# Optimization experiments

Measured on AMD Instinct MI355X. Metric: run time of the kernel, lower is better.

The kernel has to match this reference:

```python
import jax, jax.numpy as jnp
import numpy as np

BLOCKSIZE = 64
M = 8192  # out_features
N = 8192  # in_features

# bitsandbytes fp4 codebook (16 entries, normalized to [-1, 1])
FP4_CODE = np.array([0.0, 0.0052083333, 0.6666667, 1.0, 0.33333334, 0.5,
                     0.16666667, 0.25, 0.0, -0.0052083333, -0.6666667, -1.0,
                     -0.33333334, -0.5, -0.16666667, -0.25], dtype=np.float32)


def setup_inputs() -> dict:
    key = jax.random.key(0)
    k1, k2, k3, k4 = jax.random.split(key, 4)
    numel = M * N
    x = jax.random.normal(k1, (4, N), dtype=jnp.float32)
    # packed bytes: each byte holds two 4-bit codebook indices
    qweight = jax.random.randint(k2, (numel // 2,), 0, 256, dtype=jnp.int32)
    # per-block absmax scales (positive)
    absmax = jax.random.uniform(k3, (numel // BLOCKSIZE,), dtype=jnp.float32,
                                minval=0.01, maxval=1.0)
    code = jnp.asarray(FP4_CODE)
    bias = jax.random.normal(k4, (M,), dtype=jnp.float32)
    return {"x": x, "qweight": qweight, "absmax": absmax, "code": code, "bias": bias}


def _dequantize_fp4(qweight, absmax, code):
    # unpack two 4-bit indices per byte: high nibble first, low nibble second
    b = qweight.astype(jnp.int32)
    hi = (b >> 4) & 0xF
    lo = b & 0xF
    idx = jnp.stack([hi, lo], axis=-1).reshape(-1)          # [numel]
    vals = code[idx]                                        # codebook lookup
    # blockwise absmax scaling
    w = (vals.reshape(-1, BLOCKSIZE) * absmax[:, None]).reshape(M, N)
    return w


def reference(x, qweight, absmax, code, bias):
    w = _dequantize_fp4(qweight, absmax, code)              # [M, N]
    # nn.Linear semantics: y = x @ W^T + b
    return x @ w.T + bias
```

## Files before the change

kernel.cpp:

```cpp
#include <hip/hip_runtime.h>
#include <cstdint>

#define MDIM 8192
#define NDIM 8192
#define QPR  (NDIM / 2)
#define ABPR (NDIM / 64)
#define ROWS_PER_BLOCK 16
#define HGRAN 2048
#define NITER 32
#define RING 8

typedef _Float16 half2_t __attribute__((ext_vector_type(2)));
typedef uint32_t u32x4   __attribute__((ext_vector_type(4)));

__device__ __forceinline__ uint32_t f16bits(uint32_t idx) {
  uint32_t k  = idx & 7u;
  uint32_t hb = (uint32_t)(0x343138353C391D00ull >> (k * 8)) & 0xFFu;
  uint32_t lb = (0u - (hb & 1u)) & 0x55u;
  return (hb << 8) | lb | ((idx & 8u) << 12);
}

__device__ __forceinline__ uint32_t dec_pair(uint32_t b) {
  return f16bits((b >> 4) & 15u) | (f16bits(b & 15u) << 16);
}

__device__ __forceinline__ float fdot2(uint32_t w, uint32_t x, float c) {
#if __has_builtin(__builtin_amdgcn_fdot2)
  return __builtin_amdgcn_fdot2(__builtin_bit_cast(half2_t, w),
                                __builtin_bit_cast(half2_t, x), c, false);
#else
  half2_t wh = __builtin_bit_cast(half2_t, w);
  half2_t xh = __builtin_bit_cast(half2_t, x);
  return c + (float)wh.x * (float)xh.x + (float)wh.y * (float)xh.y;
#endif
}

__device__ __forceinline__ u32x4 ntload(const u32x4* p) {
#if __has_builtin(__builtin_nontemporal_load)
  return __builtin_nontemporal_load(p);
#else
  return *p;
#endif
}

__device__ __forceinline__ uint32_t swz(uint32_t g) { return g ^ ((g >> 3) & 7u); }

__global__ void bias_init(const float* __restrict__ bias, float* __restrict__ out) {
  int i = blockIdx.x * 256 + threadIdx.x;
  out[i] = bias[i & (MDIM - 1)];
}

__global__ __launch_bounds__(256, 4) void fp4gemv(
    const float* __restrict__ x, const uint32_t* __restrict__ qw,
    const float* __restrict__ am, const float* __restrict__ bias,
    float* __restrict__ out) {
  __shared__ uint32_t xs[HGRAN * 4];
  __shared__ float amx[ROWS_PER_BLOCK * 65];

  const int half = blockIdx.x & 1;
  const int mblk = blockIdx.x >> 1;

#pragma unroll 4
  for (int it = 0; it < 8; ++it) {
    int p = threadIdx.x + it * 256;
    int c = 2 * (half * HGRAN + p);
    float2 v0 = *(const float2*)(x + 0 * NDIM + c);
    float2 v1 = *(const float2*)(x + 1 * NDIM + c);
    float2 v2 = *(const float2*)(x + 2 * NDIM + c);
    float2 v3 = *(const float2*)(x + 3 * NDIM + c);
    union { _Float16 h[2]; uint32_t u; } c0, c1, c2, c3;
    c0.h[0] = (_Float16)v0.x; c0.h[1] = (_Float16)v0.y;
    c1.h[0] = (_Float16)v1.x; c1.h[1] = (_Float16)v1.y;
    c2.h[0] = (_Float16)v2.x; c2.h[1] = (_Float16)v2.y;
    c3.h[0] = (_Float16)v3.x; c3.h[1] = (_Float16)v3.y;
    uint4 w; w.x = c0.u; w.y = c1.u; w.z = c2.u; w.w = c3.u;
    *(uint4*)&xs[swz((uint32_t)p) * 4] = w;
  }
  {
    int idx = threadIdx.x * 4;
    int r = idx >> 6, j = idx & 63;
    const float* ap = am + (size_t)(mblk * ROWS_PER_BLOCK + r) * ABPR + half * 64 + j;
    float4 v = *(const float4*)ap;
    amx[r * 65 + j + 0] = v.x;
    amx[r * 65 + j + 1] = v.y;
    amx[r * 65 + j + 2] = v.z;
    amx[r * 65 + j + 3] = v.w;
  }
  __syncthreads();

  const int lane = threadIdx.x & 63;
  const int wv   = threadIdx.x >> 6;
  const int t    = lane & 15;
  const int g    = lane >> 4;
  const int rloc = wv * 4 + g;
  const int m    = mblk * ROWS_PER_BLOCK + rloc;

  const u32x4* qrow = (const u32x4*)(qw + (size_t)m * QPR + half * 2048);
  const float* arow = amx + rloc * 65 + (t >> 3);

  float a0 = 0.f, a1 = 0.f, a2 = 0.f, a3 = 0.f;

  u32x4 q[RING];
#pragma unroll
  for (int i = 0; i < RING; ++i) q[i] = ntload(&qrow[t + 16 * i]);

#pragma unroll 8
  for (int k = 0; k < NITER; ++k) {
    const int r = k & (RING - 1);
    u32x4 qA = q[r];
    int kn = k + RING; if (kn > NITER - 1) kn = NITER - 1;
    q[r] = ntload(&qrow[t + 16 * kn]);
    float sA = arow[2 * k];

    uint32_t h0 = dec_pair(qA.x);
    uint32_t h1 = dec_pair(qA.y);
    uint32_t h2 = dec_pair(qA.z);
    uint32_t h3 = dec_pair(qA.w);

    const int j0 = 4 * t + 64 * k;
    uint4 x0 = *(const uint4*)&xs[swz((uint32_t)(j0 + 0)) * 4];
    uint4 x1 = *(const uint4*)&xs[swz((uint32_t)(j0 + 1)) * 4];
    uint4 x2 = *(const uint4*)&xs[swz((uint32_t)(j0 + 2)) * 4];
    uint4 x3 = *(const uint4*)&xs[swz((uint32_t)(j0 + 3)) * 4];

    float s0, s1, s2, s3;
    s0 = fdot2(h0, x0.x, 0.f); s0 = fdot2(h1, x1.x, s0);
    s0 = fdot2(h2, x2.x, s0);  s0 = fdot2(h3, x3.x, s0);
    s1 = fdot2(h0, x0.y, 0.f); s1 = fdot2(h1, x1.y, s1);
    s1 = fdot2(h2, x2.y, s1);  s1 = fdot2(h3, x3.y, s1);
    s2 = fdot2(h0, x0.z, 0.f); s2 = fdot2(h1, x1.z, s2);
    s2 = fdot2(h2, x2.z, s2);  s2 = fdot2(h3, x3.z, s2);
    s3 = fdot2(h0, x0.w, 0.f); s3 = fdot2(h1, x1.w, s3);
    s3 = fdot2(h2, x2.w, s3);  s3 = fdot2(h3, x3.w, s3);

    a0 = fmaf(sA, s0, a0); a1 = fmaf(sA, s1, a1);
    a2 = fmaf(sA, s2, a2); a3 = fmaf(sA, s3, a3);
  }

#pragma unroll
  for (int off = 8; off > 0; off >>= 1) {
    a0 += __shfl_xor(a0, off);
    a1 += __shfl_xor(a1, off);
    a2 += __shfl_xor(a2, off);
    a3 += __shfl_xor(a3, off);
  }
  if (t == 0) {
    atomicAdd(&out[0 * MDIM + m], a0);
    atomicAdd(&out[1 * MDIM + m], a1);
    atomicAdd(&out[2 * MDIM + m], a2);
    atomicAdd(&out[3 * MDIM + m], a3);
  }
}

extern "C" void kernel_launch(void* const* d_in, const int* in_sizes, int n_in,
                              void* d_out, int out_size, void* d_ws, size_t ws_size,
                              hipStream_t stream) {
  const float*    x    = (const float*)d_in[0];
  const uint32_t* qwp  = (const uint32_t*)d_in[1];
  const float*    am   = (const float*)d_in[2];
  const float*    bias = (const float*)d_in[4];
  float*          out  = (float*)d_out;

  bias_init<<<dim3((4 * MDIM) / 256), dim3(256), 0, stream>>>(bias, out);
  fp4gemv<<<dim3((MDIM / ROWS_PER_BLOCK) * 2), dim3(256), 0, stream>>>(
      x, qwp, am, bias, out);
}
```

Before: 203.9 us.

## Have each wavefront process four rows jointly, sharing x loads across rows

Changes the work mapping so that each wavefront's 64 lanes cover a 1 KB contiguous chunk across all four of its rows, instead of 16 lanes per row. Each x fragment read from LDS is now reused for four weight rows, cutting LDS traffic per FLOP by about four. The weight-prefetch ring now interleaves rows, and the final reduction is a full 64-lane shuffle per accumulator (16 accumulators × 6 steps). This raises register pressure and adds reduction cost at the end of the kernel.

```diff
diff --git a/kernel.cpp b/kernel.cpp
--- a/kernel.cpp
+++ b/kernel.cpp
@@ -7,8 +7,7 @@
 #define ABPR (NDIM / 64)
 #define ROWS_PER_BLOCK 16
 #define HGRAN 2048
-#define NITER 32
-#define RING 8
+#define CHUNKS 8
 
 typedef _Float16 half2_t __attribute__((ext_vector_type(2)));
 typedef uint32_t u32x4   __attribute__((ext_vector_type(4)));
@@ -90,65 +89,82 @@
 
   const int lane = threadIdx.x & 63;
   const int wv   = threadIdx.x >> 6;
-  const int t    = lane & 15;
-  const int g    = lane >> 4;
-  const int rloc = wv * 4 + g;
-  const int m    = mblk * ROWS_PER_BLOCK + rloc;
+  const int m0   = mblk * ROWS_PER_BLOCK + wv * 4;
 
-  const u32x4* qrow = (const u32x4*)(qw + (size_t)m * QPR + half * 2048);
-  const float* arow = amx + rloc * 65 + (t >> 3);
+  const u32x4* qb0 = (const u32x4*)(qw + (size_t)(m0 + 0) * QPR + half * 2048);
+  const u32x4* qb1 = (const u32x4*)(qw + (size_t)(m0 + 1) * QPR + half * 2048);
+  const u32x4* qb2 = (const u32x4*)(qw + (size_t)(m0 + 2) * QPR + half * 2048);
+  const u32x4* qb3 = (const u32x4*)(qw + (size_t)(m0 + 3) * QPR + half * 2048);
 
-  float a0 = 0.f, a1 = 0.f, a2 = 0.f, a3 = 0.f;
+  float acc[4][4];
+#pragma unroll
+  for (int j = 0; j < 4; ++j)
+#pragma unroll
+    for (int b = 0; b < 4; ++b) acc[j][b] = 0.f;
 
-  u32x4 q[RING];
+  u32x4 ring[8];
+  ring[0] = ntload(&qb0[lane]);        ring[1] = ntload(&qb1[lane]);
+  ring[2] = ntload(&qb2[lane]);        ring[3] = ntload(&qb3[lane]);
+  ring[4] = ntload(&qb0[64 + lane]);   ring[5] = ntload(&qb1[64 + lane]);
+  ring[6] = ntload(&qb2[64 + lane]);   ring[7] = ntload(&qb3[64 + lane]);
+
 #pragma unroll
-  for (int i = 0; i < RING; ++i) q[i] = ntload(&qrow[t + 16 * i]);
+  for (int k = 0; k < CHUNKS; ++k) {
+    const int g0 = 256 * k + 4 * lane;
+    uint4 x0 = *(const uint4*)&xs[swz((uint32_t)(g0 + 0)) * 4];
+    uint4 x1 = *(const uint4*)&xs[swz((uint32_t)(g0 + 1)) * 4];
+    uint4 x2 = *(const uint4*)&xs[swz((uint32_t)(g0 + 2)) * 4];
+    uint4 x3 = *(const uint4*)&xs[swz((uint32_t)(g0 + 3)) * 4];
 
-#pragma unroll 8
-  for (int k = 0; k < NITER; ++k) {
-    const int r = k & (RING - 1);
-    u32x4 qA = q[r];
-    int kn = k + RING; if (kn > NITER - 1) kn = NITER - 1;
-    q[r] = ntload(&qrow[t + 16 * kn]);
-    float sA = arow[2 * k];
+    const int sb = 8 * k + (lane >> 3);
+    const int kp = (k + 2 < CHUNKS) ? k + 2 : CHUNKS - 1;
 
-    uint32_t h0 = dec_pair(qA.x);
-    uint32_t h1 = dec_pair(qA.y);
-    uint32_t h2 = dec_pair(qA.z);
-    uint32_t h3 = dec_pair(qA.w);
+#pragma unroll
+    for (int j = 0; j < 4; ++j) {
+      const int r = (4 * k + j) & 7;
+      u32x4 qA = ring[r];
+      const u32x4* qbj = (j == 0) ? qb0 : (j == 1) ? qb1 : (j == 2) ? qb2 : qb3;
+      ring[r] = ntload(&qbj[64 * kp + lane]);
 
-    const int j0 = 4 * t + 64 * k;
-    uint4 x0 = *(const uint4*)&xs[swz((uint32_t)(j0 + 0)) * 4];
-    uint4 x1 = *(const uint4*)&xs[swz((uint32_t)(j0 + 1)) * 4];
-    uint4 x2 = *(const uint4*)&xs[swz((uint32_t)(j0 + 2)) * 4];
-    uint4 x3 = *(const uint4*)&xs[swz((uint32_t)(j0 + 3)) * 4];
+      uint32_t h0 = dec_pair(qA.x);
+      uint32_t h1 = dec_pair(qA.y);
+      uint32_t h2 = dec_pair(qA.z);
+      uint32_t h3 = dec_pair(qA.w);
 
-    float s0, s1, s2, s3;
-    s0 = fdot2(h0, x0.x, 0.f); s0 = fdot2(h1, x1.x, s0);
-    s0 = fdot2(h2, x2.x, s0);  s0 = fdot2(h3, x3.x, s0);
-    s1 = fdot2(h0, x0.y, 0.f); s1 = fdot2(h1, x1.y, s1);
-    s1 = fdot2(h2, x2.y, s1);  s1 = fdot2(h3, x3.y, s1);
-    s2 = fdot2(h0, x0.z, 0.f); s2 = fdot2(h1, x1.z, s2);
-    s2 = fdot2(h2, x2.z, s2);  s2 = fdot2(h3, x3.z, s2);
-    s3 = fdot2(h0, x0.w, 0.f); s3 = fdot2(h1, x1.w, s3);
-    s3 = fdot2(h2, x2.w, s3);  s3 = fdot2(h3, x3.w, s3);
+      float sA = amx[(wv * 4 + j) * 65 + sb];
 
-    a0 = fmaf(sA, s0, a0); a1 = fmaf(sA, s1, a1);
-    a2 = fmaf(sA, s2, a2); a3 = fmaf(sA, s3, a3);
+      float t0, t1, t2, t3;
+      t0 = fdot2(h0, x0.x, 0.f); t0 = fdot2(h1, x1.x, t0);
+      t0 = fdot2(h2, x2.x, t0);  t0 = fdot2(h3, x3.x, t0);
+      t1 = fdot2(h0, x0.y, 0.f); t1 = fdot2(h1, x1.y, t1);
+      t1 = fdot2(h2, x2.y, t1);  t1 = fdot2(h3, x3.y, t1);
+      t2 = fdot2(h0, x0.z, 0.f); t2 = fdot2(h1, x1.z, t2);
+      t2 = fdot2(h2, x2.z, t2);  t2 = fdot2(h3, x3.z, t2);
+      t3 = fdot2(h0, x0.w, 0.f); t3 = fdot2(h1, x1.w, t3);
+      t3 = fdot2(h2, x2.w, t3);  t3 = fdot2(h3, x3.w, t3);
+
+      acc[j][0] = fmaf(sA, t0, acc[j][0]);
+      acc[j][1] = fmaf(sA, t1, acc[j][1]);
+      acc[j][2] = fmaf(sA, t2, acc[j][2]);
+      acc[j][3] = fmaf(sA, t3, acc[j][3]);
+    }
   }
 
 #pragma unroll
-  for (int off = 8; off > 0; off >>= 1) {
-    a0 += __shfl_xor(a0, off);
-    a1 += __shfl_xor(a1, off);
-    a2 += __shfl_xor(a2, off);
-    a3 += __shfl_xor(a3, off);
-  }
-  if (t == 0) {
-    atomicAdd(&out[0 * MDIM + m], a0);
-    atomicAdd(&out[1 * MDIM + m], a1);
-    atomicAdd(&out[2 * MDIM + m], a2);
-    atomicAdd(&out[3 * MDIM + m], a3);
+  for (int j = 0; j < 4; ++j)
+#pragma unroll
+    for (int b = 0; b < 4; ++b)
+#pragma unroll
+      for (int off = 32; off > 0; off >>= 1)
+        acc[j][b] += __shfl_xor(acc[j][b], off);
+
+  if (lane == 0) {
+#pragma unroll
+    for (int j = 0; j < 4; ++j) {
+#pragma unroll
+      for (int b = 0; b < 4; ++b)
+        atomicAdd(&out[b * MDIM + (m0 + j)], acc[j][b]);
+    }
   }
 }
 
```

Measured after the change: 200.3 us. About the same (-1.8%).
